# Performance work log

Hardware: AMD Instinct MI355X
Metric: run time of the kernel (lower is better)

## Reference

```python
import jax, jax.numpy as jnp
import numpy as np

jax.config.update("jax_enable_x64", True)


def setup_inputs() -> dict:
    H = 131072          # num_hints
    N = 1_048_576       # number of DB entries (rows of `entries`)
    BLOCK = 1024        # block_size; blocks and offsets both in [0, BLOCK)
    MAXSZ = 128         # per-hint subset size in [1, MAXSZ)
    rng = np.random.default_rng(0)

    sizes = rng.integers(1, MAXSZ, size=H)               # ragged segment sizes
    starts = np.concatenate([[0], np.cumsum(sizes)[:-1]])  # CSR exclusive prefix
    T = int(sizes.sum())                                  # ~8.4M total indices

    blocks = rng.integers(0, BLOCK, size=T)
    offsets = rng.integers(0, BLOCK, size=T)
    entries = rng.integers(0, 2**62, size=(N, 5), dtype=np.int64)

    return {
        "entries": jnp.asarray(entries, dtype=jnp.int64),
        "subset_blocks": jnp.asarray(blocks, dtype=jnp.int64),
        "subset_offsets": jnp.asarray(offsets, dtype=jnp.int64),
        "subset_starts": jnp.asarray(starts, dtype=jnp.int64),
        "subset_sizes": jnp.asarray(sizes, dtype=jnp.int64),
        "block_size": BLOCK,
    }


def reference(entries, subset_blocks, subset_offsets, subset_starts, subset_sizes, block_size):
    """Gather + variable-length segment XOR reduction.

    entries:        [N, 5] int64
    subset_blocks:  [T]    int64 flat ragged buffer
    subset_offsets: [T]    int64 flat ragged buffer
    subset_starts:  [H]    int64 CSR-style start of each hint's slice
    subset_sizes:   [H]    int64 length of each hint's slice
    returns:        [H, 5] int64 XOR parities (zeros for empty hints)
    """
    n = entries.shape[0]
    idx = jnp.clip(subset_blocks * block_size + subset_offsets, 0, n - 1)  # [T]
    selected = entries[idx]                                                # [T, 5]

    # Prefix-XOR along the flat token axis; XOR is associative so
    # segment XOR = cum[start+size] ^ cum[start] with cum[0] = 0.
    cum = jax.lax.associative_scan(jnp.bitwise_xor, selected, axis=0)      # [T, 5]
    cum = jnp.concatenate([jnp.zeros((1, 5), dtype=entries.dtype), cum], axis=0)

    ends = subset_starts + subset_sizes
    parities = jnp.bitwise_xor(cum[ends], cum[subset_starts])              # [H, 5]
    return parities
```

## Files before the change

### kernel.cpp

```cpp
#include <hip/hip_runtime.h>


#define HPG     256
#define NSL     16
#define LDS_CAP 19456

__device__ __forceinline__ int clip_idx(int v, int N) {
    return min(max(v, 0), N - 1);
}

__global__ __launch_bounds__(256) void bucket_kernel(
    const int* __restrict__ blocks,
    const int* __restrict__ offsets,
    const int* __restrict__ starts,
    const int* __restrict__ bs_ptr,
    const int* __restrict__ entries,
    int* __restrict__ out,
    unsigned short* __restrict__ bIdxLo,
    unsigned char*  __restrict__ bHint,
    unsigned int*   __restrict__ chunkTab,
    unsigned int*   __restrict__ cursor,
    int H, int N, int T)
{
    __shared__ unsigned int w[LDS_CAP];
    __shared__ int lstart[HPG + 1];
    __shared__ unsigned int cnt[NSL], lbase[NSL], lcur[NSL];

    const int g  = blockIdx.x;
    const int t  = threadIdx.x;
    const int h0 = g * HPG;
    const int h1 = min(H, h0 + HPG);
    const int nh = h1 - h0;
    const int bs = bs_ptr[0];

    for (int i = t; i < nh; i += 256) lstart[i] = starts[h0 + i];
    if (t == 0) lstart[nh] = (h1 < H) ? starts[h1] : T;
    if (t < NSL) { cnt[t] = 0; lcur[t] = 0; }
    __syncthreads();

    const int tokBase = lstart[0];
    const int count   = lstart[nh] - tokBase;
    const int staged  = min(count, LDS_CAP);

    for (int i = t; i < staged; i += 256) {
        int b = blocks[tokBase + i];
        int o = offsets[tokBase + i];
        int idx = clip_idx(b * bs + o, N);
        unsigned int s = (unsigned int)idx >> 16;
        w[i] = (unsigned int)(idx & 0xFFFF) | (s << 24);
        atomicAdd(&cnt[s], 1u);
    }
    __syncthreads();

    if (t < nh) {
        int lo = lstart[t] - tokBase;
        int hi = min(lstart[t + 1] - tokBase, staged);
        for (int i = lo; i < hi; ++i) w[i] |= ((unsigned int)t << 16);
    }
    __syncthreads();

    if (t < NSL) {
        unsigned int base = atomicAdd(cursor, cnt[t]);
        lbase[t] = base;
        chunkTab[(g * NSL + t) * 2 + 0] = base;
        chunkTab[(g * NSL + t) * 2 + 1] = cnt[t];
    }
    __syncthreads();

    for (int i = t; i < staged; i += 256) {
        unsigned int wd = w[i];
        unsigned int s  = wd >> 24;
        unsigned int r  = atomicAdd(&lcur[s], 1u);
        unsigned int p  = lbase[s] + r;
        bIdxLo[p] = (unsigned short)(wd & 0xFFFF);
        bHint[p]  = (unsigned char)((wd >> 16) & 0xFF);
    }

    for (int i = staged + t; i < count; i += 256) {
        int b = blocks[tokBase + i];
        int o = offsets[tokBase + i];
        int idx = clip_idx(b * bs + o, N);
        int gpos = tokBase + i;
        int lo = 0, hi = nh - 1;
        while (lo < hi) {
            int m = (lo + hi + 1) >> 1;
            if (lstart[m] <= gpos) lo = m; else hi = m - 1;
        }
        const int* row = entries + (long)idx * 5;
        int* o5 = out + (long)(h0 + lo) * 5;
        atomicXor(&o5[0], row[0]); atomicXor(&o5[1], row[1]);
        atomicXor(&o5[2], row[2]); atomicXor(&o5[3], row[3]);
        atomicXor(&o5[4], row[4]);
    }
}

__global__ __launch_bounds__(256) void gather_kernel(
    const unsigned short* __restrict__ bIdxLo,
    const unsigned char*  __restrict__ bHint,
    const unsigned int*   __restrict__ chunkTab,
    const int* __restrict__ entries,
    int* __restrict__ out,
    int H, int NG, int nSl, int groupsPerBlock)
{
    __shared__ int acc[HPG * 5];
    const int B = blockIdx.x;
    const int x = B & 7;
    const int g0 = B >> 3;
    const int t = threadIdx.x;
    const int gStride = gridDim.x >> 3;

    for (int k = 0; k < groupsPerBlock; ++k) {
        const int g = g0 + k * gStride;
        if (g >= NG) break;

        for (int i = t; i < HPG * 5; i += 256) acc[i] = 0;
        __syncthreads();

        for (int s = x; s < nSl; s += 8) {
            const unsigned int base = chunkTab[(g * NSL + s) * 2 + 0];
            const unsigned int cn   = chunkTab[(g * NSL + s) * 2 + 1];
            const int hiBits = s << 16;
            for (unsigned int i = t; i < cn; i += 256) {
                int idx = hiBits | (int)bIdxLo[base + i];
                int h   = (int)bHint[base + i];
                const int* row = entries + (long)idx * 5;
                atomicXor(&acc[h * 5 + 0], row[0]);
                atomicXor(&acc[h * 5 + 1], row[1]);
                atomicXor(&acc[h * 5 + 2], row[2]);
                atomicXor(&acc[h * 5 + 3], row[3]);
                atomicXor(&acc[h * 5 + 4], row[4]);
            }
        }
        __syncthreads();

        const long obase = (long)g * HPG * 5;
        const long omax  = (long)H * 5;
        for (int i = t; i < HPG * 5; i += 256) {
            if (obase + i < omax && acc[i] != 0)
                atomicXor(&out[obase + i], acc[i]);
        }
        __syncthreads();
    }
}

__global__ __launch_bounds__(256) void hint_xor_wave(
    const int* __restrict__ entries,
    const int* __restrict__ blocks,
    const int* __restrict__ offsets,
    const int* __restrict__ starts,
    const int* __restrict__ sizes,
    const int* __restrict__ bs_ptr,
    int* __restrict__ out,
    int H, int N)
{
    const int gtid = blockIdx.x * blockDim.x + threadIdx.x;
    const int hint = gtid >> 6;
    const int lane = gtid & 63;
    if (hint >= H) return;

    const int start = starts[hint];
    const int size  = sizes[hint];
    const int bs    = bs_ptr[0];

    int a0 = 0, a1 = 0, a2 = 0, a3 = 0, a4 = 0;
    for (int j = lane; j < size; j += 64) {
        int idx = clip_idx(blocks[start + j] * bs + offsets[start + j], N);
        const int* row = entries + (size_t)idx * 5;
        a0 ^= row[0]; a1 ^= row[1]; a2 ^= row[2]; a3 ^= row[3]; a4 ^= row[4];
    }
    #pragma unroll
    for (int m = 1; m < 64; m <<= 1) {
        a0 ^= __shfl_xor(a0, m);
        a1 ^= __shfl_xor(a1, m);
        a2 ^= __shfl_xor(a2, m);
        a3 ^= __shfl_xor(a3, m);
        a4 ^= __shfl_xor(a4, m);
    }
    if (lane == 0) {
        int* o = out + (size_t)hint * 5;
        o[0] = a0; o[1] = a1; o[2] = a2; o[3] = a3; o[4] = a4;
    }
}

extern "C" void kernel_launch(void* const* d_in, const int* in_sizes, int n_in,
                              void* d_out, int out_size, void* d_ws, size_t ws_size,
                              hipStream_t stream) {
    const int* entries = (const int*)d_in[0];
    const int* blocks  = (const int*)d_in[1];
    const int* offsets = (const int*)d_in[2];
    const int* starts  = (const int*)d_in[3];
    const int* sizes   = (const int*)d_in[4];
    const int* bs      = (const int*)d_in[5];
    int* out = (int*)d_out;

    const int H = in_sizes[3];
    const int T = in_sizes[1];
    const int N = in_sizes[0] / 5;

    const int NG  = (H + HPG - 1) / HPG;
    const int nSl = (N + 65535) >> 16;

    const size_t cursorOff = 0;
    const size_t tabOff    = 64;
    const size_t loOff     = tabOff + (size_t)NG * NSL * 2 * 4;
    const size_t hOff      = loOff + (size_t)T * 2;
    const size_t need      = hOff + (size_t)T + 64;

    const bool ok = (N <= (1 << 20)) && (nSl <= NSL) && (ws_size >= need) &&
                    (NG >= 8);

    if (ok) {
        unsigned int*   cursor   = (unsigned int*)((char*)d_ws + cursorOff);
        unsigned int*   chunkTab = (unsigned int*)((char*)d_ws + tabOff);
        unsigned short* bIdxLo   = (unsigned short*)((char*)d_ws + loOff);
        unsigned char*  bHint    = (unsigned char*)((char*)d_ws + hOff);

        hipMemsetAsync(d_out, 0, (size_t)out_size * sizeof(int), stream);
        hipMemsetAsync(cursor, 0, sizeof(unsigned int), stream);

        hipLaunchKernelGGL(bucket_kernel, dim3(NG), dim3(256), 0, stream,
                           blocks, offsets, starts, bs, entries, out,
                           bIdxLo, bHint, chunkTab, cursor, H, N, T);

        int gridB = 2048;
        if (gridB > NG * 8) gridB = NG * 8;
        const int gStride = gridB >> 3;
        const int gpb = (NG + gStride - 1) / gStride;

        hipLaunchKernelGGL(gather_kernel, dim3(gridB), dim3(256), 0, stream,
                           bIdxLo, bHint, chunkTab, entries, out,
                           H, NG, nSl, gpb);
    } else {
        const long total_threads = (long)H * 64;
        const int block = 256;
        const int grid = (int)((total_threads + block - 1) / block);
        hipLaunchKernelGGL(hint_xor_wave, dim3(grid), dim3(block), 0, stream,
                           entries, blocks, offsets, starts, sizes, bs, out, H, N);
    }
}
```

Before: 220.8 us.

## Replace LDS-staged bucketing with fixed-capacity global buckets and packed 64-bit LDS XOR

The bucket kernel no longer stages tokens in LDS and no longer uses a global cursor to build compacted buckets. It now uses 1024 threads per group, does a binary search per token to find its hint, and takes a global atomic rank into a fixed-capacity slot for each (group, slice) pair. Tokens past the slot capacity fall back to direct global atomic XOR. The gather kernel loads each 5-int row with paired int2 loads and accumulates with two 64-bit LDS atomics plus one 32-bit atomic, where it previously used five 32-bit atomics. In exchange the change adds heavy global atomic contention on the count table, a larger sparse workspace, and per-token binary search.

```diff
diff --git a/kernel.cpp b/kernel.cpp
--- a/kernel.cpp
+++ b/kernel.cpp
@@ -1,15 +1,35 @@
 #include <hip/hip_runtime.h>
 
 
-#define HPG     256
-#define NSL     16
-#define LDS_CAP 19456
+#define HPG  256
+#define NSL  16
+#define CAP  1344
 
 __device__ __forceinline__ int clip_idx(int v, int N) {
     return min(max(v, 0), N - 1);
 }
 
-__global__ __launch_bounds__(256) void bucket_kernel(
+__device__ __forceinline__ unsigned long long pk64(int lo, int hi) {
+    return (unsigned long long)(unsigned int)lo |
+           ((unsigned long long)(unsigned int)hi << 32);
+}
+
+__device__ __forceinline__ void load_row5(const int* __restrict__ e, int idx,
+                                          int& e0, int& e1, int& e2, int& e3, int& e4) {
+    const int d0 = idx * 5;
+    const bool even = (idx & 1) == 0;
+    const int pairBase = even ? (d0 >> 1) : ((d0 + 1) >> 1);
+    int2 u = ((const int2*)e)[pairBase];
+    int2 v = ((const int2*)e)[pairBase + 1];
+    int  w = e[even ? d0 + 4 : d0];
+    e0 = even ? u.x : w;
+    e1 = even ? u.y : u.x;
+    e2 = even ? v.x : u.y;
+    e3 = even ? v.y : v.x;
+    e4 = even ? w   : v.y;
+}
+
+__global__ __launch_bounds__(1024) void bucket_kernel(
     const int* __restrict__ blocks,
     const int* __restrict__ offsets,
     const int* __restrict__ starts,
@@ -18,13 +38,10 @@
     int* __restrict__ out,
     unsigned short* __restrict__ bIdxLo,
     unsigned char*  __restrict__ bHint,
-    unsigned int*   __restrict__ chunkTab,
-    unsigned int*   __restrict__ cursor,
+    unsigned int*   __restrict__ tabCnt,
     int H, int N, int T)
 {
-    __shared__ unsigned int w[LDS_CAP];
     __shared__ int lstart[HPG + 1];
-    __shared__ unsigned int cnt[NSL], lbase[NSL], lcur[NSL];
 
     const int g  = blockIdx.x;
     const int t  = threadIdx.x;
@@ -33,76 +50,51 @@
     const int nh = h1 - h0;
     const int bs = bs_ptr[0];
 
-    for (int i = t; i < nh; i += 256) lstart[i] = starts[h0 + i];
+    if (t < nh) lstart[t] = starts[h0 + t];
     if (t == 0) lstart[nh] = (h1 < H) ? starts[h1] : T;
-    if (t < NSL) { cnt[t] = 0; lcur[t] = 0; }
     __syncthreads();
 
     const int tokBase = lstart[0];
     const int count   = lstart[nh] - tokBase;
-    const int staged  = min(count, LDS_CAP);
-
-    for (int i = t; i < staged; i += 256) {
-        int b = blocks[tokBase + i];
-        int o = offsets[tokBase + i];
-        int idx = clip_idx(b * bs + o, N);
-        unsigned int s = (unsigned int)idx >> 16;
-        w[i] = (unsigned int)(idx & 0xFFFF) | (s << 24);
-        atomicAdd(&cnt[s], 1u);
-    }
-    __syncthreads();
-
-    if (t < nh) {
-        int lo = lstart[t] - tokBase;
-        int hi = min(lstart[t + 1] - tokBase, staged);
-        for (int i = lo; i < hi; ++i) w[i] |= ((unsigned int)t << 16);
-    }
-    __syncthreads();
-
-    if (t < NSL) {
-        unsigned int base = atomicAdd(cursor, cnt[t]);
-        lbase[t] = base;
-        chunkTab[(g * NSL + t) * 2 + 0] = base;
-        chunkTab[(g * NSL + t) * 2 + 1] = cnt[t];
-    }
-    __syncthreads();
-
-    for (int i = t; i < staged; i += 256) {
-        unsigned int wd = w[i];
-        unsigned int s  = wd >> 24;
-        unsigned int r  = atomicAdd(&lcur[s], 1u);
-        unsigned int p  = lbase[s] + r;
-        bIdxLo[p] = (unsigned short)(wd & 0xFFFF);
-        bHint[p]  = (unsigned char)((wd >> 16) & 0xFF);
-    }
-
-    for (int i = staged + t; i < count; i += 256) {
-        int b = blocks[tokBase + i];
-        int o = offsets[tokBase + i];
-        int idx = clip_idx(b * bs + o, N);
-        int gpos = tokBase + i;
+
+    for (int i = t; i < count; i += 1024) {
+        const int gpos = tokBase + i;
+        const int idx  = clip_idx(blocks[gpos] * bs + offsets[gpos], N);
+        const unsigned int s = (unsigned int)idx >> 16;
+
         int lo = 0, hi = nh - 1;
         while (lo < hi) {
             int m = (lo + hi + 1) >> 1;
             if (lstart[m] <= gpos) lo = m; else hi = m - 1;
         }
-        const int* row = entries + (long)idx * 5;
-        int* o5 = out + (long)(h0 + lo) * 5;
-        atomicXor(&o5[0], row[0]); atomicXor(&o5[1], row[1]);
-        atomicXor(&o5[2], row[2]); atomicXor(&o5[3], row[3]);
-        atomicXor(&o5[4], row[4]);
+
+        const unsigned int rank = atomicAdd(&tabCnt[g * NSL + s], 1u);
+        if (rank < CAP) {
+            const size_t p = ((size_t)(g * NSL + s)) * CAP + rank;
+            bIdxLo[p] = (unsigned short)(idx & 0xFFFF);
+            bHint[p]  = (unsigned char)lo;
+        } else {
+            int e0, e1, e2, e3, e4;
+            load_row5(entries, idx, e0, e1, e2, e3, e4);
+            int* o5 = out + (long)(h0 + lo) * 5;
+            atomicXor(&o5[0], e0); atomicXor(&o5[1], e1);
+            atomicXor(&o5[2], e2); atomicXor(&o5[3], e3);
+            atomicXor(&o5[4], e4);
+        }
     }
 }
 
 __global__ __launch_bounds__(256) void gather_kernel(
     const unsigned short* __restrict__ bIdxLo,
     const unsigned char*  __restrict__ bHint,
-    const unsigned int*   __restrict__ chunkTab,
+    const unsigned int*   __restrict__ tabCnt,
     const int* __restrict__ entries,
     int* __restrict__ out,
     int H, int NG, int nSl, int groupsPerBlock)
 {
-    __shared__ int acc[HPG * 5];
+    __shared__ unsigned long long accLL[HPG * 2];
+    __shared__ int acc4[HPG];
+
     const int B = blockIdx.x;
     const int x = B & 7;
     const int g0 = B >> 3;
@@ -113,31 +105,43 @@
         const int g = g0 + k * gStride;
         if (g >= NG) break;
 
-        for (int i = t; i < HPG * 5; i += 256) acc[i] = 0;
+        for (int i = t; i < HPG * 2; i += 256) accLL[i] = 0ull;
+        for (int i = t; i < HPG; i += 256) acc4[i] = 0;
         __syncthreads();
 
         for (int s = x; s < nSl; s += 8) {
-            const unsigned int base = chunkTab[(g * NSL + s) * 2 + 0];
-            const unsigned int cn   = chunkTab[(g * NSL + s) * 2 + 1];
+            const unsigned int cn =
+                min(tabCnt[g * NSL + s], (unsigned int)CAP);
+            const size_t base = ((size_t)(g * NSL + s)) * CAP;
             const int hiBits = s << 16;
             for (unsigned int i = t; i < cn; i += 256) {
-                int idx = hiBits | (int)bIdxLo[base + i];
-                int h   = (int)bHint[base + i];
-                const int* row = entries + (long)idx * 5;
-                atomicXor(&acc[h * 5 + 0], row[0]);
-                atomicXor(&acc[h * 5 + 1], row[1]);
-                atomicXor(&acc[h * 5 + 2], row[2]);
-                atomicXor(&acc[h * 5 + 3], row[3]);
-                atomicXor(&acc[h * 5 + 4], row[4]);
+                const int idx = hiBits | (int)bIdxLo[base + i];
+                const int h   = (int)bHint[base + i];
+                int e0, e1, e2, e3, e4;
+                load_row5(entries, idx, e0, e1, e2, e3, e4);
+                atomicXor(&accLL[h * 2 + 0], pk64(e0, e1));
+                atomicXor(&accLL[h * 2 + 1], pk64(e2, e3));
+                atomicXor(&acc4[h], e4);
             }
         }
         __syncthreads();
 
         const long obase = (long)g * HPG * 5;
         const long omax  = (long)H * 5;
-        for (int i = t; i < HPG * 5; i += 256) {
-            if (obase + i < omax && acc[i] != 0)
-                atomicXor(&out[obase + i], acc[i]);
+        for (int h = t; h < HPG; h += 256) {
+            const long o = obase + (long)h * 5;
+            if (o + 4 < omax || o < omax) {
+                unsigned long long v01 = accLL[h * 2 + 0];
+                unsigned long long v23 = accLL[h * 2 + 1];
+                int a0 = (int)(unsigned int)v01, a1 = (int)(unsigned int)(v01 >> 32);
+                int a2 = (int)(unsigned int)v23, a3 = (int)(unsigned int)(v23 >> 32);
+                int a4 = acc4[h];
+                if (o + 0 < omax && a0) atomicXor(&out[o + 0], a0);
+                if (o + 1 < omax && a1) atomicXor(&out[o + 1], a1);
+                if (o + 2 < omax && a2) atomicXor(&out[o + 2], a2);
+                if (o + 3 < omax && a3) atomicXor(&out[o + 3], a3);
+                if (o + 4 < omax && a4) atomicXor(&out[o + 4], a4);
+            }
         }
         __syncthreads();
     }
@@ -200,27 +204,26 @@
     const int NG  = (H + HPG - 1) / HPG;
     const int nSl = (N + 65535) >> 16;
 
-    const size_t cursorOff = 0;
-    const size_t tabOff    = 64;
-    const size_t loOff     = tabOff + (size_t)NG * NSL * 2 * 4;
-    const size_t hOff      = loOff + (size_t)T * 2;
-    const size_t need      = hOff + (size_t)T + 64;
-
-    const bool ok = (N <= (1 << 20)) && (nSl <= NSL) && (ws_size >= need) &&
-                    (NG >= 8);
+    const size_t tabOff = 0;
+    const size_t tabBytes = (size_t)NG * NSL * sizeof(unsigned int);
+    const size_t loOff  = (tabOff + tabBytes + 63) & ~(size_t)63;
+    const size_t loBytes = (size_t)NG * NSL * CAP * sizeof(unsigned short);
+    const size_t hOff   = loOff + loBytes;
+    const size_t need   = hOff + (size_t)NG * NSL * CAP + 64;
+
+    const bool ok = (N <= (1 << 20)) && (nSl <= NSL) && (ws_size >= need);
 
     if (ok) {
-        unsigned int*   cursor   = (unsigned int*)((char*)d_ws + cursorOff);
-        unsigned int*   chunkTab = (unsigned int*)((char*)d_ws + tabOff);
-        unsigned short* bIdxLo   = (unsigned short*)((char*)d_ws + loOff);
-        unsigned char*  bHint    = (unsigned char*)((char*)d_ws + hOff);
+        unsigned int*   tabCnt = (unsigned int*)((char*)d_ws + tabOff);
+        unsigned short* bIdxLo = (unsigned short*)((char*)d_ws + loOff);
+        unsigned char*  bHint  = (unsigned char*)((char*)d_ws + hOff);
 
         hipMemsetAsync(d_out, 0, (size_t)out_size * sizeof(int), stream);
-        hipMemsetAsync(cursor, 0, sizeof(unsigned int), stream);
-
-        hipLaunchKernelGGL(bucket_kernel, dim3(NG), dim3(256), 0, stream,
+        hipMemsetAsync(tabCnt, 0, tabBytes, stream);
+
+        hipLaunchKernelGGL(bucket_kernel, dim3(NG), dim3(1024), 0, stream,
                            blocks, offsets, starts, bs, entries, out,
-                           bIdxLo, bHint, chunkTab, cursor, H, N, T);
+                           bIdxLo, bHint, tabCnt, H, N, T);
 
         int gridB = 2048;
         if (gridB > NG * 8) gridB = NG * 8;
@@ -228,7 +231,7 @@
         const int gpb = (NG + gStride - 1) / gStride;
 
         hipLaunchKernelGGL(gather_kernel, dim3(gridB), dim3(256), 0, stream,
-                           bIdxLo, bHint, chunkTab, entries, out,
+                           bIdxLo, bHint, tabCnt, entries, out,
                            H, NG, nSl, gpb);
     } else {
         const long total_threads = (long)H * 64;
```

Measured after the change: 437.5 us. 1.98x slower.

## Pack bucket entries into 32-bit words with in-place offsets and smaller hint groups

Applied to the files above, without the earlier changes.

Bucketed entries become one packed 32-bit word per token (20-bit row index, hint id in the upper bits) instead of separate 16-bit index and 8-bit hint arrays. Each group now writes its buckets into its own token range using a local prefix sum, which removes the global cursor atomic and its memset. The hint group size drops to 128 with 1024-thread bucket blocks, and each token's hint is found by binary search instead of a per-hint fill loop. This trades more bucket write traffic and per-token search work for simpler, more coalesced gather loads and more gather blocks.

```diff
diff --git a/kernel.cpp b/kernel.cpp
--- a/kernel.cpp
+++ b/kernel.cpp
@@ -1,30 +1,28 @@
 #include <hip/hip_runtime.h>
 
 
-#define HPG     256
-#define NSL     16
-#define LDS_CAP 19456
+#define HPG        128
+#define NSL        16
+#define STAGE_CAP  12288
 
 __device__ __forceinline__ int clip_idx(int v, int N) {
     return min(max(v, 0), N - 1);
 }
 
-__global__ __launch_bounds__(256) void bucket_kernel(
+__global__ __launch_bounds__(1024) void bucket_kernel(
     const int* __restrict__ blocks,
     const int* __restrict__ offsets,
     const int* __restrict__ starts,
     const int* __restrict__ bs_ptr,
     const int* __restrict__ entries,
     int* __restrict__ out,
-    unsigned short* __restrict__ bIdxLo,
-    unsigned char*  __restrict__ bHint,
-    unsigned int*   __restrict__ chunkTab,
-    unsigned int*   __restrict__ cursor,
+    unsigned int* __restrict__ buck,
+    unsigned int* __restrict__ tab,
     int H, int N, int T)
 {
-    __shared__ unsigned int w[LDS_CAP];
+    __shared__ unsigned int stage[STAGE_CAP];
     __shared__ int lstart[HPG + 1];
-    __shared__ unsigned int cnt[NSL], lbase[NSL], lcur[NSL];
+    __shared__ unsigned int cnt[NSL], off[NSL], lcur[NSL];
 
     const int g  = blockIdx.x;
     const int t  = threadIdx.x;
@@ -33,54 +31,49 @@
     const int nh = h1 - h0;
     const int bs = bs_ptr[0];
 
-    for (int i = t; i < nh; i += 256) lstart[i] = starts[h0 + i];
+    if (t < nh) lstart[t] = starts[h0 + t];
     if (t == 0) lstart[nh] = (h1 < H) ? starts[h1] : T;
     if (t < NSL) { cnt[t] = 0; lcur[t] = 0; }
     __syncthreads();
 
     const int tokBase = lstart[0];
     const int count   = lstart[nh] - tokBase;
-    const int staged  = min(count, LDS_CAP);
-
-    for (int i = t; i < staged; i += 256) {
-        int b = blocks[tokBase + i];
-        int o = offsets[tokBase + i];
-        int idx = clip_idx(b * bs + o, N);
-        unsigned int s = (unsigned int)idx >> 16;
-        w[i] = (unsigned int)(idx & 0xFFFF) | (s << 24);
-        atomicAdd(&cnt[s], 1u);
+    const int staged  = min(count, STAGE_CAP);
+
+    for (int i = t; i < staged; i += 1024) {
+        const int gpos = tokBase + i;
+        const int idx  = clip_idx(blocks[gpos] * bs + offsets[gpos], N);
+        int lo = 0, hi = nh - 1;
+        while (lo < hi) {
+            int m = (lo + hi + 1) >> 1;
+            if (lstart[m] <= gpos) lo = m; else hi = m - 1;
+        }
+        stage[i] = (unsigned int)idx | ((unsigned int)lo << 20);
+        atomicAdd(&cnt[(unsigned int)idx >> 16], 1u);
     }
     __syncthreads();
 
-    if (t < nh) {
-        int lo = lstart[t] - tokBase;
-        int hi = min(lstart[t + 1] - tokBase, staged);
-        for (int i = lo; i < hi; ++i) w[i] |= ((unsigned int)t << 16);
+    if (t == 0) {
+        unsigned int run = 0;
+        for (int s = 0; s < NSL; ++s) { off[s] = run; run += cnt[s]; }
     }
     __syncthreads();
 
     if (t < NSL) {
-        unsigned int base = atomicAdd(cursor, cnt[t]);
-        lbase[t] = base;
-        chunkTab[(g * NSL + t) * 2 + 0] = base;
-        chunkTab[(g * NSL + t) * 2 + 1] = cnt[t];
-    }
-    __syncthreads();
-
-    for (int i = t; i < staged; i += 256) {
-        unsigned int wd = w[i];
-        unsigned int s  = wd >> 24;
-        unsigned int r  = atomicAdd(&lcur[s], 1u);
-        unsigned int p  = lbase[s] + r;
-        bIdxLo[p] = (unsigned short)(wd & 0xFFFF);
-        bHint[p]  = (unsigned char)((wd >> 16) & 0xFF);
-    }
-
-    for (int i = staged + t; i < count; i += 256) {
-        int b = blocks[tokBase + i];
-        int o = offsets[tokBase + i];
-        int idx = clip_idx(b * bs + o, N);
-        int gpos = tokBase + i;
+        tab[(g * NSL + t) * 2 + 0] = (unsigned int)tokBase + off[t];
+        tab[(g * NSL + t) * 2 + 1] = cnt[t];
+    }
+
+    for (int i = t; i < staged; i += 1024) {
+        const unsigned int w = stage[i];
+        const unsigned int s = (w >> 16) & (NSL - 1);
+        const unsigned int r = atomicAdd(&lcur[s], 1u);
+        buck[(unsigned int)tokBase + off[s] + r] = w;
+    }
+
+    for (int i = staged + t; i < count; i += 1024) {
+        const int gpos = tokBase + i;
+        const int idx  = clip_idx(blocks[gpos] * bs + offsets[gpos], N);
         int lo = 0, hi = nh - 1;
         while (lo < hi) {
             int m = (lo + hi + 1) >> 1;
@@ -95,14 +88,14 @@
 }
 
 __global__ __launch_bounds__(256) void gather_kernel(
-    const unsigned short* __restrict__ bIdxLo,
-    const unsigned char*  __restrict__ bHint,
-    const unsigned int*   __restrict__ chunkTab,
+    const unsigned int* __restrict__ buck,
+    const unsigned int* __restrict__ tab,
     const int* __restrict__ entries,
     int* __restrict__ out,
     int H, int NG, int nSl, int groupsPerBlock)
 {
     __shared__ int acc[HPG * 5];
+
     const int B = blockIdx.x;
     const int x = B & 7;
     const int g0 = B >> 3;
@@ -117,12 +110,12 @@
         __syncthreads();
 
         for (int s = x; s < nSl; s += 8) {
-            const unsigned int base = chunkTab[(g * NSL + s) * 2 + 0];
-            const unsigned int cn   = chunkTab[(g * NSL + s) * 2 + 1];
-            const int hiBits = s << 16;
+            const unsigned int base = tab[(g * NSL + s) * 2 + 0];
+            const unsigned int cn   = tab[(g * NSL + s) * 2 + 1];
             for (unsigned int i = t; i < cn; i += 256) {
-                int idx = hiBits | (int)bIdxLo[base + i];
-                int h   = (int)bHint[base + i];
+                const unsigned int w = buck[base + i];
+                const int idx = (int)(w & 0xFFFFFu);
+                const int h   = (int)(w >> 20);
                 const int* row = entries + (long)idx * 5;
                 atomicXor(&acc[h * 5 + 0], row[0]);
                 atomicXor(&acc[h * 5 + 1], row[1]);
@@ -136,8 +129,11 @@
         const long obase = (long)g * HPG * 5;
         const long omax  = (long)H * 5;
         for (int i = t; i < HPG * 5; i += 256) {
-            if (obase + i < omax && acc[i] != 0)
-                atomicXor(&out[obase + i], acc[i]);
+            const long o = obase + i;
+            if (o < omax) {
+                const int v = acc[i];
+                if (v) atomicXor(&out[o], v);
+            }
         }
         __syncthreads();
     }
@@ -200,36 +196,31 @@
     const int NG  = (H + HPG - 1) / HPG;
     const int nSl = (N + 65535) >> 16;
 
-    const size_t cursorOff = 0;
-    const size_t tabOff    = 64;
-    const size_t loOff     = tabOff + (size_t)NG * NSL * 2 * 4;
-    const size_t hOff      = loOff + (size_t)T * 2;
-    const size_t need      = hOff + (size_t)T + 64;
+    const size_t buckOff  = 0;
+    const size_t buckBytes = (size_t)T * 4;
+    const size_t tabOff   = (buckOff + buckBytes + 63) & ~(size_t)63;
+    const size_t need     = tabOff + (size_t)NG * NSL * 2 * 4 + 64;
 
     const bool ok = (N <= (1 << 20)) && (nSl <= NSL) && (ws_size >= need) &&
-                    (NG >= 8);
+                    (H <= (1 << 27));
 
     if (ok) {
-        unsigned int*   cursor   = (unsigned int*)((char*)d_ws + cursorOff);
-        unsigned int*   chunkTab = (unsigned int*)((char*)d_ws + tabOff);
-        unsigned short* bIdxLo   = (unsigned short*)((char*)d_ws + loOff);
-        unsigned char*  bHint    = (unsigned char*)((char*)d_ws + hOff);
+        unsigned int* buck = (unsigned int*)((char*)d_ws + buckOff);
+        unsigned int* tab  = (unsigned int*)((char*)d_ws + tabOff);
 
         hipMemsetAsync(d_out, 0, (size_t)out_size * sizeof(int), stream);
-        hipMemsetAsync(cursor, 0, sizeof(unsigned int), stream);
-
-        hipLaunchKernelGGL(bucket_kernel, dim3(NG), dim3(256), 0, stream,
+
+        hipLaunchKernelGGL(bucket_kernel, dim3(NG), dim3(1024), 0, stream,
                            blocks, offsets, starts, bs, entries, out,
-                           bIdxLo, bHint, chunkTab, cursor, H, N, T);
+                           buck, tab, H, N, T);
 
         int gridB = 2048;
         if (gridB > NG * 8) gridB = NG * 8;
-        const int gStride = gridB >> 3;
+        const int gStride = (gridB >= 8) ? (gridB >> 3) : 1;
         const int gpb = (NG + gStride - 1) / gStride;
 
         hipLaunchKernelGGL(gather_kernel, dim3(gridB), dim3(256), 0, stream,
-                           bIdxLo, bHint, chunkTab, entries, out,
-                           H, NG, nSl, gpb);
+                           buck, tab, entries, out, H, NG, nSl, gpb);
     } else {
         const long total_threads = (long)H * 64;
         const int block = 256;
```

Result: faster. 189.1 us (-14.3%).
